# Kernel optimization log

Hardware: AMD Instinct MI355X
Metric: run time of the kernel (lower is better)

Reference implementation:

```python
import jax, jax.numpy as jnp
import numpy as np

B = 128            # fixed by min(128, len(sample)) loop
NODES_PER_GRAPH = 100
N_NODES = B * NODES_PER_GRAPH
HID = 512          # args.num_hidden
EMB = 1024         # pretrained embedding dim (t_linear in_features)
TWEET_VOCAB = 300000
DESC_VOCAB = 150000
EPS = 1e-5


def setup_inputs() -> dict:
    key = jax.random.key(0)
    ks = jax.random.split(key, 12)
    sample = jnp.stack([
        jax.random.randint(ks[0], (B,), 0, DESC_VOCAB),
        jax.random.randint(ks[1], (B,), 0, TWEET_VOCAB),
        jax.random.randint(ks[2], (B,), 0, DESC_VOCAB),
    ], axis=1)  # [B,3] int
    # sorted node->graph assignment; every graph has >=2 nodes so u_idx+1 is valid
    graph_batch = jnp.repeat(jnp.arange(B), NODES_PER_GRAPH)  # [N_NODES]
    p_feature = jax.random.normal(ks[3], (N_NODES, HID), dtype=jnp.float32)
    tweet_emb = jax.random.normal(ks[4], (TWEET_VOCAB, EMB), dtype=jnp.float32) * 0.02
    desc_emb = jax.random.normal(ks[5], (DESC_VOCAB, EMB), dtype=jnp.float32) * 0.02
    t_w = jax.random.normal(ks[6], (HID, EMB), dtype=jnp.float32) / np.sqrt(EMB)
    t_b = jnp.zeros((HID,), dtype=jnp.float32)
    w1 = jax.random.normal(ks[7], (256, 3 * HID), dtype=jnp.float32) / np.sqrt(3 * HID)
    b1 = jnp.zeros((256,), dtype=jnp.float32)
    gamma = jnp.ones((256,), dtype=jnp.float32)
    beta = jnp.zeros((256,), dtype=jnp.float32)
    w2 = jax.random.normal(ks[8], (1, 256), dtype=jnp.float32) / np.sqrt(256)
    b2 = jnp.zeros((1,), dtype=jnp.float32)
    return {"sample": sample, "graph_batch": graph_batch, "p_feature": p_feature,
            "tweet_emb": tweet_emb, "desc_emb": desc_emb, "t_w": t_w, "t_b": t_b,
            "w1": w1, "b1": b1, "gamma": gamma, "beta": beta, "w2": w2, "b2": b2}


def reference(sample, graph_batch, p_feature, tweet_emb, desc_emb,
              t_w, t_b, w1, b1, gamma, beta, w2, b2):
    # torch.nonzero(batch == i)[0] -> first node index of graph i;
    # graph_batch is sorted, so this is a searchsorted (replaces the 128-iter loop)
    u_idx = jnp.searchsorted(graph_batch, jnp.arange(B))  # [B]
    v_idx = u_idx + 1
    u_feat = p_feature[u_idx]  # [B, HID]
    v_feat = p_feature[v_idx]  # [B, HID]

    t = lambda e: e @ t_w.T + t_b  # Linear(1024 -> HID)
    inp = jnp.concatenate([
        u_feat + t(desc_emb[sample[:, 0]]),
        t(tweet_emb[sample[:, 1]]),
        v_feat + t(desc_emb[sample[:, 2]]),
    ], axis=1)  # [B, 3*HID]

    h = inp @ w1.T + b1  # [B, 256]
    # BatchNorm1d in training mode: biased batch statistics
    mu = jnp.mean(h, axis=0)
    var = jnp.mean((h - mu) ** 2, axis=0)
    h = (h - mu) * jax.lax.rsqrt(var + EPS) * gamma + beta
    # Dropout treated as identity (eval / deterministic reference)
    h = jax.nn.relu(h)
    return jax.nn.sigmoid(h @ w2.T + b2)  # [B, 1]
```

## Files before the change

### kernel.cpp

```cpp
#include <hip/hip_runtime.h>
#include <math.h>

#define HID 512
#define EMB 1024
#define N1 1536
#define N2 256
#define P2S (128 * 256)

typedef __attribute__((ext_vector_type(8))) __bf16 bf16x8;
typedef __attribute__((ext_vector_type(4))) __bf16 bf16x4;
typedef __attribute__((ext_vector_type(4))) float fx4;

#define OFF_ABUF 0
#define OFF_TWB  786432
#define OFF_W1B  1835008
#define OFF_INPB 2621440
#define OFF_P2   3014656
#define OFF_UIDX 3538944

__device__ __forceinline__ fx4 mfma16(bf16x8 a, bf16x8 b, fx4 c) {
    return __builtin_amdgcn_mfma_f32_16x16x32_bf16(a, b, c, 0, 0, 0);
}

__global__ __launch_bounds__(256)
void kPrep(const int* __restrict__ sample, const int* __restrict__ gb, int n_nodes,
           const float* __restrict__ tweet_emb, const float* __restrict__ desc_emb,
           const float* __restrict__ t_w, const float* __restrict__ w1,
           __bf16* __restrict__ Abuf, __bf16* __restrict__ twb,
           __bf16* __restrict__ w1b, int* __restrict__ uidx)
{
    const int blk = blockIdx.x;
    const int t   = threadIdx.x;

    if (blk < 384) {
        const int s = blk >> 7, b = blk & 127;
        const int id = sample[b * 3 + s];
        const float* src = (s == 1) ? (tweet_emb + (size_t)id * EMB)
                                    : (desc_emb + (size_t)id * EMB);
        float4 v = *(const float4*)(src + t * 4);
        bf16x4 o = {(__bf16)v.x, (__bf16)v.y, (__bf16)v.z, (__bf16)v.w};
        *(bf16x4*)(Abuf + (size_t)blk * EMB + t * 4) = o;
    } else if (blk < 896) {
        const int r = blk - 384;
        float4 v = *(const float4*)(t_w + (size_t)r * EMB + t * 4);
        bf16x4 o = {(__bf16)v.x, (__bf16)v.y, (__bf16)v.z, (__bf16)v.w};
        *(bf16x4*)(twb + (size_t)r * EMB + t * 4) = o;
    } else if (blk < 1152) {
        const int r = blk - 896;
        #pragma unroll
        for (int i = t; i < 384; i += 256) {
            float4 v = *(const float4*)(w1 + (size_t)r * N1 + i * 4);
            bf16x4 o = {(__bf16)v.x, (__bf16)v.y, (__bf16)v.z, (__bf16)v.w};
            *(bf16x4*)(w1b + (size_t)r * N1 + i * 4) = o;
        }
    } else {
        const int n = (blk - 1152) * 256 + t;
        if (n < n_nodes) {
            const int g = gb[n];
            if (n == 0 || gb[n - 1] != g) uidx[g] = n;
        }
    }
}

__global__ __launch_bounds__(256, 1)
void kG1(const __bf16* __restrict__ Abuf, const __bf16* __restrict__ twb,
         const float* __restrict__ t_b, const float* __restrict__ p_feature,
         const int* __restrict__ uidx, __bf16* __restrict__ inp_bf)
{
    const int n0 = blockIdx.x * 32;
    const int m0 = blockIdx.y * 32;
    const int t  = threadIdx.x;
    const int wid = t >> 6, l = t & 63;
    const int mbase = (wid >> 1) * 16, nbase = (wid & 1) * 16;

    __shared__ __bf16 Alds[32 * 1024];
    __shared__ __bf16 Blds[32 * 1024];

    bf16x8 areg[16], breg[16];
    #pragma unroll
    for (int i = 0; i < 16; ++i) {
        const int c = i * 256 + t;
        const int row = c >> 7, g = c & 127;
        areg[i] = *(const bf16x8*)(Abuf + (size_t)(m0 + row) * EMB + g * 8);
        breg[i] = *(const bf16x8*)(twb  + (size_t)(n0 + row) * EMB + g * 8);
    }
    #pragma unroll
    for (int i = 0; i < 16; ++i) {
        const int c = i * 256 + t;
        const int row = c >> 7, g = c & 127;
        const int gp = g ^ (row & 7);
        *(bf16x8*)(Alds + row * 1024 + gp * 8) = areg[i];
        *(bf16x8*)(Blds + row * 1024 + gp * 8) = breg[i];
    }
    __syncthreads();

    fx4 acc0 = {}, acc1 = {};
    const int fr = l & 15, fq = l >> 4;
    const __bf16* Ab = Alds + (mbase + fr) * 1024;
    const __bf16* Bb = Blds + (nbase + fr) * 1024;
    const int ax = (mbase + fr) & 7, bx = (nbase + fr) & 7;
    #pragma unroll
    for (int s = 0; s < 32; s += 2) {
        bf16x8 a0 = *(const bf16x8*)(Ab + ((s * 4 + fq) ^ ax) * 8);
        bf16x8 b0 = *(const bf16x8*)(Bb + ((s * 4 + fq) ^ bx) * 8);
        acc0 = mfma16(a0, b0, acc0);
        bf16x8 a1 = *(const bf16x8*)(Ab + (((s + 1) * 4 + fq) ^ ax) * 8);
        bf16x8 b1 = *(const bf16x8*)(Bb + (((s + 1) * 4 + fq) ^ bx) * 8);
        acc1 = mfma16(a1, b1, acc1);
    }

    const int sid  = m0 >> 7;
    const int col  = n0 + nbase + fr;
    const int row0 = m0 + mbase + fq * 4;
    const float tb = t_b[col];
    #pragma unroll
    for (int j = 0; j < 4; ++j) {
        const int r = row0 + j;
        float v = acc0[j] + acc1[j] + tb;
        if (sid != 1) {
            const int node = uidx[r & 127] + ((sid == 2) ? 1 : 0);
            v += p_feature[(size_t)node * HID + col];
        }
        inp_bf[(size_t)(r & 127) * N1 + sid * HID + col] = (__bf16)v;
    }
}

__global__ __launch_bounds__(256)
void kG2(const __bf16* __restrict__ inp_bf, const __bf16* __restrict__ w1b,
         float* __restrict__ part2)
{
    const int n0 = blockIdx.x * 32;
    const int m0 = blockIdx.y * 32;
    const int ks = blockIdx.z;
    const int t  = threadIdx.x;
    const int wid = t >> 6, l = t & 63;
    const int mbase = (wid >> 1) * 16, nbase = (wid & 1) * 16;

    __shared__ __bf16 Alds[32 * 384];
    __shared__ __bf16 Blds[32 * 384];

    bf16x8 areg[6], breg[6];
    #pragma unroll
    for (int i = 0; i < 6; ++i) {
        const int c = i * 256 + t;
        const int row = c / 48, g = c % 48;
        areg[i] = *(const bf16x8*)(inp_bf + (size_t)(m0 + row) * N1 + ks * 384 + g * 8);
        breg[i] = *(const bf16x8*)(w1b   + (size_t)(n0 + row) * N1 + ks * 384 + g * 8);
    }
    #pragma unroll
    for (int i = 0; i < 6; ++i) {
        const int c = i * 256 + t;
        const int row = c / 48, g = c % 48;
        const int gp = g ^ (row & 7);
        *(bf16x8*)(Alds + row * 384 + gp * 8) = areg[i];
        *(bf16x8*)(Blds + row * 384 + gp * 8) = breg[i];
    }
    __syncthreads();

    fx4 acc0 = {}, acc1 = {};
    const int fr = l & 15, fq = l >> 4;
    const __bf16* Ab = Alds + (mbase + fr) * 384;
    const __bf16* Bb = Blds + (nbase + fr) * 384;
    const int ax = (mbase + fr) & 7, bx = (nbase + fr) & 7;
    #pragma unroll
    for (int s = 0; s < 12; s += 2) {
        bf16x8 a0 = *(const bf16x8*)(Ab + ((s * 4 + fq) ^ ax) * 8);
        bf16x8 b0 = *(const bf16x8*)(Bb + ((s * 4 + fq) ^ bx) * 8);
        acc0 = mfma16(a0, b0, acc0);
        bf16x8 a1 = *(const bf16x8*)(Ab + (((s + 1) * 4 + fq) ^ ax) * 8);
        bf16x8 b1 = *(const bf16x8*)(Bb + (((s + 1) * 4 + fq) ^ bx) * 8);
        acc1 = mfma16(a1, b1, acc1);
    }

    float* dst = part2 + (size_t)ks * P2S;
    const int col  = n0 + nbase + fr;
    const int row0 = m0 + mbase + fq * 4;
    #pragma unroll
    for (int j = 0; j < 4; ++j)
        dst[(size_t)(row0 + j) * N2 + col] = acc0[j] + acc1[j];
}

__global__ __launch_bounds__(256)
void kEF(const float* __restrict__ part2, const float* __restrict__ b1,
         const float* __restrict__ gamma, const float* __restrict__ beta,
         const float* __restrict__ w2, const float* __restrict__ b2,
         float* __restrict__ out)
{
    __shared__ float s_scale[256];
    __shared__ float s_shift[256];
    const int t = threadIdx.x;

    const float bias = b1[t];
    float sum = 0.f, sq = 0.f;
    #pragma unroll 4
    for (int r = 0; r < 128; ++r) {
        float v = (((part2[r * N2 + t] + part2[P2S + r * N2 + t])
                  + part2[2 * P2S + r * N2 + t]) + part2[3 * P2S + r * N2 + t]) + bias;
        sum += v;
        sq  += v * v;
    }
    const float mu  = sum * (1.0f / 128.0f);
    const float var = sq * (1.0f / 128.0f) - mu * mu;
    const float rs  = rsqrtf(var + 1e-5f);
    const float sc  = gamma[t] * rs;
    s_scale[t] = sc;
    s_shift[t] = beta[t] - mu * sc;
    __syncthreads();

    const int wv = t >> 6, l = t & 63;
    #pragma unroll
    for (int rr = 0; rr < 2; ++rr) {
        const int b = blockIdx.x * 8 + wv * 2 + rr;
        float acc = 0.f;
        #pragma unroll
        for (int i = 0; i < 4; ++i) {
            const int j = l + i * 64;
            float v = (((part2[b * N2 + j] + part2[P2S + b * N2 + j])
                      + part2[2 * P2S + b * N2 + j]) + part2[3 * P2S + b * N2 + j]) + b1[j];
            float x = v * s_scale[j] + s_shift[j];
            x = fmaxf(x, 0.f);
            acc += x * w2[j];
        }
        #pragma unroll
        for (int off = 32; off; off >>= 1) acc += __shfl_xor(acc, off);
        if (l == 0) out[b] = 1.0f / (1.0f + expf(-(acc + b2[0])));
    }
}

extern "C" void kernel_launch(void* const* d_in, const int* in_sizes, int n_in,
                              void* d_out, int out_size, void* d_ws, size_t ws_size,
                              hipStream_t stream) {
    const int*   sample    = (const int*)  d_in[0];
    const int*   gb        = (const int*)  d_in[1];
    const float* p_feature = (const float*)d_in[2];
    const float* tweet_emb = (const float*)d_in[3];
    const float* desc_emb  = (const float*)d_in[4];
    const float* t_w       = (const float*)d_in[5];
    const float* t_b       = (const float*)d_in[6];
    const float* w1        = (const float*)d_in[7];
    const float* b1        = (const float*)d_in[8];
    const float* gamma     = (const float*)d_in[9];
    const float* beta      = (const float*)d_in[10];
    const float* w2        = (const float*)d_in[11];
    const float* b2        = (const float*)d_in[12];
    float* out = (float*)d_out;

    char* ws = (char*)d_ws;
    __bf16* Abuf   = (__bf16*)(ws + OFF_ABUF);
    __bf16* twb    = (__bf16*)(ws + OFF_TWB);
    __bf16* w1b    = (__bf16*)(ws + OFF_W1B);
    __bf16* inp_bf = (__bf16*)(ws + OFF_INPB);
    float*  part2  = (float*)(ws + OFF_P2);
    int*    uidx   = (int*)  (ws + OFF_UIDX);

    const int n_nodes = in_sizes[1];
    const int scatter_blocks = (n_nodes + 255) / 256;

    kPrep<<<1152 + scatter_blocks, 256, 0, stream>>>(sample, gb, n_nodes,
        tweet_emb, desc_emb, t_w, w1, Abuf, twb, w1b, uidx);
    kG1<<<dim3(16, 12), 256, 0, stream>>>(Abuf, twb, t_b, p_feature, uidx, inp_bf);
    kG2<<<dim3(8, 4, 4), 256, 0, stream>>>(inp_bf, w1b, part2);
    kEF<<<16, 256, 0, stream>>>(part2, b1, gamma, beta, w2, b2, out);
}
```

Baseline: 34.17 us.

## Split GEMM1 into split-K 64x64 tiled kernel plus separate combine kernel

The first GEMM moves from 32x32 tiles with the whole K=1024 staged in LDS to 64x64 tiles with a 4-way split-K. Each block loops over 64-wide K chunks, prefetching the next chunk into registers. Partial fp32 results go to a new workspace buffer. A new kernel sums the partials and adds the bias and p_feature before converting to bf16. This cuts LDS use and register pressure per block and raises reuse per tile, but adds a kernel launch and an fp32 round trip through global memory. A few unroll pragmas also change.

```diff
diff --git a/kernel.cpp b/kernel.cpp
--- a/kernel.cpp
+++ b/kernel.cpp
@@ -1,6 +1,7 @@
 #include <hip/hip_runtime.h>
 #include <math.h>
 
+#define BB 128
 #define HID 512
 #define EMB 1024
 #define N1 1536
@@ -15,19 +16,24 @@
 #define OFF_TWB  786432
 #define OFF_W1B  1835008
 #define OFF_INPB 2621440
-#define OFF_P2   3014656
-#define OFF_UIDX 3538944
+#define OFF_P1   3014656
+#define OFF_P2   6160384
+#define OFF_UIDX 6684672
 
 __device__ __forceinline__ fx4 mfma16(bf16x8 a, bf16x8 b, fx4 c) {
     return __builtin_amdgcn_mfma_f32_16x16x32_bf16(a, b, c, 0, 0, 0);
 }
 
-__global__ __launch_bounds__(256)
-void kPrep(const int* __restrict__ sample, const int* __restrict__ gb, int n_nodes,
-           const float* __restrict__ tweet_emb, const float* __restrict__ desc_emb,
-           const float* __restrict__ t_w, const float* __restrict__ w1,
-           __bf16* __restrict__ Abuf, __bf16* __restrict__ twb,
-           __bf16* __restrict__ w1b, int* __restrict__ uidx)
+__device__ __forceinline__ int lds_idx64(int row, int g) {
+    return row * 64 + ((g ^ (row & 7)) * 8);
+}
+
+__global__ __launch_bounds__(256)
+void kA_prep(const int* __restrict__ sample, const int* __restrict__ gb, int n_nodes,
+             const float* __restrict__ tweet_emb, const float* __restrict__ desc_emb,
+             const float* __restrict__ t_w, const float* __restrict__ w1,
+             __bf16* __restrict__ Abuf, __bf16* __restrict__ twb,
+             __bf16* __restrict__ w1b, int* __restrict__ uidx)
 {
     const int blk = blockIdx.x;
     const int t   = threadIdx.x;
@@ -47,7 +53,6 @@
         *(bf16x4*)(twb + (size_t)r * EMB + t * 4) = o;
     } else if (blk < 1152) {
         const int r = blk - 896;
-        #pragma unroll
         for (int i = t; i < 384; i += 256) {
             float4 v = *(const float4*)(w1 + (size_t)r * N1 + i * 4);
             bf16x4 o = {(__bf16)v.x, (__bf16)v.y, (__bf16)v.z, (__bf16)v.w};
@@ -62,67 +67,102 @@
     }
 }
 
-__global__ __launch_bounds__(256, 1)
-void kG1(const __bf16* __restrict__ Abuf, const __bf16* __restrict__ twb,
-         const float* __restrict__ t_b, const float* __restrict__ p_feature,
-         const int* __restrict__ uidx, __bf16* __restrict__ inp_bf)
-{
-    const int n0 = blockIdx.x * 32;
-    const int m0 = blockIdx.y * 32;
+__global__ __launch_bounds__(256)
+void kB_gemm1(const __bf16* __restrict__ Abuf, const __bf16* __restrict__ twb,
+              float* __restrict__ part1)
+{
+    const int n0 = blockIdx.x * 64;
+    const int m0 = blockIdx.y * 64;
+    const int ks = blockIdx.z;
     const int t  = threadIdx.x;
     const int wid = t >> 6, l = t & 63;
-    const int mbase = (wid >> 1) * 16, nbase = (wid & 1) * 16;
-
-    __shared__ __bf16 Alds[32 * 1024];
-    __shared__ __bf16 Blds[32 * 1024];
-
-    bf16x8 areg[16], breg[16];
-    #pragma unroll
-    for (int i = 0; i < 16; ++i) {
-        const int c = i * 256 + t;
-        const int row = c >> 7, g = c & 127;
-        areg[i] = *(const bf16x8*)(Abuf + (size_t)(m0 + row) * EMB + g * 8);
-        breg[i] = *(const bf16x8*)(twb  + (size_t)(n0 + row) * EMB + g * 8);
-    }
-    #pragma unroll
-    for (int i = 0; i < 16; ++i) {
-        const int c = i * 256 + t;
-        const int row = c >> 7, g = c & 127;
-        const int gp = g ^ (row & 7);
-        *(bf16x8*)(Alds + row * 1024 + gp * 8) = areg[i];
-        *(bf16x8*)(Blds + row * 1024 + gp * 8) = breg[i];
-    }
-    __syncthreads();
-
-    fx4 acc0 = {}, acc1 = {};
-    const int fr = l & 15, fq = l >> 4;
-    const __bf16* Ab = Alds + (mbase + fr) * 1024;
-    const __bf16* Bb = Blds + (nbase + fr) * 1024;
-    const int ax = (mbase + fr) & 7, bx = (nbase + fr) & 7;
-    #pragma unroll
-    for (int s = 0; s < 32; s += 2) {
-        bf16x8 a0 = *(const bf16x8*)(Ab + ((s * 4 + fq) ^ ax) * 8);
-        bf16x8 b0 = *(const bf16x8*)(Bb + ((s * 4 + fq) ^ bx) * 8);
-        acc0 = mfma16(a0, b0, acc0);
-        bf16x8 a1 = *(const bf16x8*)(Ab + (((s + 1) * 4 + fq) ^ ax) * 8);
-        bf16x8 b1 = *(const bf16x8*)(Bb + (((s + 1) * 4 + fq) ^ bx) * 8);
-        acc1 = mfma16(a1, b1, acc1);
-    }
-
-    const int sid  = m0 >> 7;
-    const int col  = n0 + nbase + fr;
-    const int row0 = m0 + mbase + fq * 4;
-    const float tb = t_b[col];
-    #pragma unroll
-    for (int j = 0; j < 4; ++j) {
-        const int r = row0 + j;
-        float v = acc0[j] + acc1[j] + tb;
-        if (sid != 1) {
-            const int node = uidx[r & 127] + ((sid == 2) ? 1 : 0);
-            v += p_feature[(size_t)node * HID + col];
-        }
-        inp_bf[(size_t)(r & 127) * N1 + sid * HID + col] = (__bf16)v;
-    }
+    const int mbase = (wid >> 1) * 32, nbase = (wid & 1) * 32;
+
+    __shared__ __bf16 Alds[64 * 64];
+    __shared__ __bf16 Blds[64 * 64];
+
+    const int srow = t >> 2;
+    const int g0   = (t & 3) * 2;
+
+    fx4 acc[2][2] = {};
+
+    bf16x8 av0, av1, bv0, bv1;
+    {
+        const int k0 = ks * 256;
+        const __bf16* ap = Abuf + (size_t)(m0 + srow) * EMB + k0 + g0 * 8;
+        const __bf16* bp = twb  + (size_t)(n0 + srow) * EMB + k0 + g0 * 8;
+        av0 = *(const bf16x8*)ap; av1 = *(const bf16x8*)(ap + 8);
+        bv0 = *(const bf16x8*)bp; bv1 = *(const bf16x8*)(bp + 8);
+    }
+
+    for (int kt = 0; kt < 4; ++kt) {
+        __syncthreads();
+        *(bf16x8*)&Alds[lds_idx64(srow, g0)]     = av0;
+        *(bf16x8*)&Alds[lds_idx64(srow, g0 + 1)] = av1;
+        *(bf16x8*)&Blds[lds_idx64(srow, g0)]     = bv0;
+        *(bf16x8*)&Blds[lds_idx64(srow, g0 + 1)] = bv1;
+        __syncthreads();
+
+        if (kt < 3) {
+            const int k0 = ks * 256 + (kt + 1) * 64;
+            const __bf16* ap = Abuf + (size_t)(m0 + srow) * EMB + k0 + g0 * 8;
+            const __bf16* bp = twb  + (size_t)(n0 + srow) * EMB + k0 + g0 * 8;
+            av0 = *(const bf16x8*)ap; av1 = *(const bf16x8*)(ap + 8);
+            bv0 = *(const bf16x8*)bp; bv1 = *(const bf16x8*)(bp + 8);
+        }
+
+        #pragma unroll
+        for (int kq = 0; kq < 2; ++kq) {
+            const int g = kq * 4 + (l >> 4);
+            bf16x8 a0 = *(const bf16x8*)&Alds[lds_idx64(mbase +      (l & 15), g)];
+            bf16x8 a1 = *(const bf16x8*)&Alds[lds_idx64(mbase + 16 + (l & 15), g)];
+            bf16x8 b0 = *(const bf16x8*)&Blds[lds_idx64(nbase +      (l & 15), g)];
+            bf16x8 b1 = *(const bf16x8*)&Blds[lds_idx64(nbase + 16 + (l & 15), g)];
+            acc[0][0] = mfma16(a0, b0, acc[0][0]);
+            acc[0][1] = mfma16(a0, b1, acc[0][1]);
+            acc[1][0] = mfma16(a1, b0, acc[1][0]);
+            acc[1][1] = mfma16(a1, b1, acc[1][1]);
+        }
+    }
+
+    float* dst = part1 + (size_t)ks * (384 * 512);
+    #pragma unroll
+    for (int mi = 0; mi < 2; ++mi)
+        #pragma unroll
+        for (int ni = 0; ni < 2; ++ni) {
+            const int row = m0 + mbase + mi * 16 + (l >> 4) * 4;
+            const int col = n0 + nbase + ni * 16 + (l & 15);
+            #pragma unroll
+            for (int j = 0; j < 4; ++j)
+                dst[(size_t)(row + j) * 512 + col] = acc[mi][ni][j];
+        }
+}
+
+__global__ __launch_bounds__(256)
+void kC_comb1(const float* __restrict__ part1, const float* __restrict__ t_b,
+              const float* __restrict__ p_feature, const int* __restrict__ uidx,
+              __bf16* __restrict__ inp_bf)
+{
+    const int t = threadIdx.x;
+    const int m = blockIdx.x * 2 + (t >> 7);
+    const int j0 = (t & 127) * 4;
+    const int s = m >> 7, b = m & 127;
+
+    float4 v = *(const float4*)(part1 + (size_t)m * 512 + j0);
+    #pragma unroll
+    for (int p = 1; p < 4; ++p) {
+        float4 q = *(const float4*)(part1 + (size_t)p * (384 * 512) + (size_t)m * 512 + j0);
+        v.x += q.x; v.y += q.y; v.z += q.z; v.w += q.w;
+    }
+    float4 tb = *(const float4*)(t_b + j0);
+    v.x += tb.x; v.y += tb.y; v.z += tb.z; v.w += tb.w;
+    if (s != 1) {
+        const int node = (s == 0) ? uidx[b] : (uidx[b] + 1);
+        float4 pf = *(const float4*)(p_feature + (size_t)node * HID + j0);
+        v.x += pf.x; v.y += pf.y; v.z += pf.z; v.w += pf.w;
+    }
+    bf16x4 o = {(__bf16)v.x, (__bf16)v.y, (__bf16)v.z, (__bf16)v.w};
+    *(bf16x4*)(inp_bf + (size_t)b * N1 + s * HID + j0) = o;
 }
 
 __global__ __launch_bounds__(256)
@@ -192,7 +232,7 @@
 
     const float bias = b1[t];
     float sum = 0.f, sq = 0.f;
-    #pragma unroll 4
+    #pragma unroll 8
     for (int r = 0; r < 128; ++r) {
         float v = (((part2[r * N2 + t] + part2[P2S + r * N2 + t])
                   + part2[2 * P2S + r * N2 + t]) + part2[3 * P2S + r * N2 + t]) + bias;
@@ -250,15 +290,17 @@
     __bf16* twb    = (__bf16*)(ws + OFF_TWB);
     __bf16* w1b    = (__bf16*)(ws + OFF_W1B);
     __bf16* inp_bf = (__bf16*)(ws + OFF_INPB);
+    float*  part1  = (float*)(ws + OFF_P1);
     float*  part2  = (float*)(ws + OFF_P2);
     int*    uidx   = (int*)  (ws + OFF_UIDX);
 
     const int n_nodes = in_sizes[1];
     const int scatter_blocks = (n_nodes + 255) / 256;
 
-    kPrep<<<1152 + scatter_blocks, 256, 0, stream>>>(sample, gb, n_nodes,
+    kA_prep<<<1152 + scatter_blocks, 256, 0, stream>>>(sample, gb, n_nodes,
         tweet_emb, desc_emb, t_w, w1, Abuf, twb, w1b, uidx);
-    kG1<<<dim3(16, 12), 256, 0, stream>>>(Abuf, twb, t_b, p_feature, uidx, inp_bf);
+    kB_gemm1<<<dim3(8, 6, 4), 256, 0, stream>>>(Abuf, twb, part1);
+    kC_comb1<<<192, 256, 0, stream>>>(part1, t_b, p_feature, uidx, inp_bf);
     kG2<<<dim3(8, 4, 4), 256, 0, stream>>>(inp_bf, w1b, part2);
     kEF<<<16, 256, 0, stream>>>(part2, b1, gamma, beta, w2, b2, out);
 }
```

After: 32.31 us. 1.06x faster.
